# Optimization experiments

Measured on AMD Instinct MI355X. Metric: run time of the kernel, lower is better.

Reference implementation:

```python
import jax, jax.numpy as jnp
import numpy as np

B, R, N, D, H = 32, 5, 1024, 256, 256

def setup_inputs() -> dict:
    key = jax.random.key(0)
    k1, k2, k3, k4 = jax.random.split(key, 4)
    nodes = jax.random.normal(k1, (B, N, D), dtype=jnp.float32)
    adj = jax.random.uniform(k2, (B, R, N, N), dtype=jnp.float32)
    # kaiming_normal_ approximation: std = sqrt(2 / fan_in)
    std = np.sqrt(2.0 / D).astype(np.float32)
    w_0 = jax.random.normal(k3, (H, D), dtype=jnp.float32) * std
    w_r = jax.random.normal(k4, (R, H, D), dtype=jnp.float32) * std
    return {"nodes": nodes, "adj": adj, "w_0": w_0, "w_r": w_r}

def reference(nodes, adj, w_0, w_r):
    # nodes: (B,N,D), adj: (B,R,N,N), w_0: (H,D), w_r: (R,H,D)
    xw_0 = jnp.einsum('bnd,hd->bnh', nodes, w_0)            # (B,N,H)
    xw_r = jnp.einsum('bnd,rhd->brnh', nodes, w_r)          # (B,R,N,H)
    c_r = jnp.sum(adj, axis=-1, keepdims=True)              # (B,R,N,1)
    c_r = jnp.where(c_r == 0, jnp.ones_like(c_r), c_r)
    out = jnp.sum(xw_r / c_r, axis=1) + xw_0                # (B,N,H)
    # dropout is identity in eval mode
    return out
```

## Files before the change

kernel.cpp:

```cpp
#include <hip/hip_runtime.h>
#include <hip/hip_bf16.h>


#define BB 32
#define RR 5
#define NN 1024
#define DD 256
#define HH 256
#define MM (BB * NN)

typedef __attribute__((ext_vector_type(8))) short short8;
typedef __attribute__((ext_vector_type(4))) float f32x4;

#define GAS(p) ((const __attribute__((address_space(1))) void*)(p))
#define LAS(p) ((__attribute__((address_space(3))) void*)(p))

__device__ __forceinline__ unsigned short f2bf(float f) {
    unsigned int u = __float_as_uint(f);
    unsigned int r = (u + 0x7FFFu + ((u >> 16) & 1u)) >> 16;
    return (unsigned short)r;
}

__global__ void cvt_kernel(const float* __restrict__ in,
                           unsigned short* __restrict__ out, int n) {
    int i = (blockIdx.x * blockDim.x + threadIdx.x) * 4;
    if (i >= n) return;
    float4 v = *reinterpret_cast<const float4*>(in + i);
    ushort4 o;
    o.x = f2bf(v.x); o.y = f2bf(v.y); o.z = f2bf(v.z); o.w = f2bf(v.w);
    *reinterpret_cast<ushort4*>(out + i) = o;
}

__global__ __launch_bounds__(256) void rowsum_kernel(const float* __restrict__ adj,
                                                     float* __restrict__ inv_c) {
    const int wave = blockIdx.x * 4 + (threadIdx.x >> 6);
    const int lane = threadIdx.x & 63;
    const float4* row4 = reinterpret_cast<const float4*>(adj + (size_t)wave * NN);
    float s = 0.f;
#pragma unroll
    for (int i = 0; i < 4; ++i) {
        float4 v = row4[lane + 64 * i];
        s += (v.x + v.y) + (v.z + v.w);
    }
#pragma unroll
    for (int off = 32; off > 0; off >>= 1) s += __shfl_down(s, off, 64);
    if (lane == 0) {
        float c = (s == 0.f) ? 1.f : s;
        inv_c[wave] = 1.f / c;
    }
}

__global__ __launch_bounds__(256) void gemm_kernel(
    const unsigned short* __restrict__ nodesb,
    const unsigned short* __restrict__ wb,
    const float* __restrict__ inv_c,
    float* __restrict__ out) {
    __shared__ unsigned short smem[14336];
    __shared__ float s_inv[RR * 64];

    const int tid  = threadIdx.x;
    const int lane = tid & 63;
    const int wv   = tid >> 6;
    const int row_base = blockIdx.x * 64;
    const int col_base = blockIdx.y * 64;
    const int m    = lane & 15;
    const int quad = lane >> 4;

    const unsigned short* gp[7];
    unsigned short*       lp[7];
#pragma unroll
    for (int j = 0; j < 7; ++j) {
        const int c = wv * 7 + j;
        lp[j] = smem + c * 512;
        if (c < 4) {
            const int u   = c * 64 + lane;
            const int row = u >> 2;
            const int kc  = u & 3;
            gp[j] = nodesb + (size_t)(row_base + row) * DD + kc * 8;
        } else {
            const int u    = (c - 4) * 64 + lane;
            const int col6 = u >> 2;
            const int kc   = u & 3;
            const int set  = col6 >> 6;
            const int col  = col6 & 63;
            gp[j] = wb + (size_t)(set * HH + col_base + col) * DD + kc * 8;
        }
    }

    f32x4 acc[6][4];
#pragma unroll
    for (int s = 0; s < 6; ++s)
#pragma unroll
        for (int t = 0; t < 4; ++t) acc[s][t] = (f32x4){0.f, 0.f, 0.f, 0.f};

    const unsigned short* aL = smem + m * 32 + quad * 8;
    const unsigned short* bL = smem + 2048 + (wv * 16 + m) * 32 + quad * 8;

    for (int kt = 0; kt < 8; ++kt) {
        __syncthreads();
#pragma unroll
        for (int j = 0; j < 7; ++j)
            __builtin_amdgcn_global_load_lds(GAS(gp[j] + kt * 32), LAS(lp[j]), 16, 0, 0);
        __syncthreads();

        short8 afr[4];
#pragma unroll
        for (int t = 0; t < 4; ++t)
            afr[t] = *reinterpret_cast<const short8*>(aL + t * 512);
#pragma unroll
        for (int s = 0; s < 6; ++s) {
            short8 bfr = *reinterpret_cast<const short8*>(bL + s * 2048);
#pragma unroll
            for (int t = 0; t < 4; ++t)
                acc[s][t] = __builtin_amdgcn_mfma_f32_16x16x32_bf16(afr[t], bfr, acc[s][t], 0, 0, 0);
        }
    }

    const int b  = row_base >> 10;
    const int n0 = row_base & (NN - 1);
    __syncthreads();
#pragma unroll
    for (int i = tid; i < RR * 64; i += 256) {
        const int r = i >> 6, nl = i & 63;
        s_inv[i] = inv_c[((size_t)b * RR + r) * NN + n0 + nl];
    }
    __syncthreads();

    const int hcol = col_base + wv * 16 + m;
#pragma unroll
    for (int t = 0; t < 4; ++t) {
#pragma unroll
        for (int i = 0; i < 4; ++i) {
            const int rloc = t * 16 + quad * 4 + i;
            float v = acc[0][t][i];
#pragma unroll
            for (int r = 0; r < RR; ++r)
                v += s_inv[r * 64 + rloc] * acc[r + 1][t][i];
            out[(size_t)(row_base + rloc) * HH + hcol] = v;
        }
    }
}

extern "C" void kernel_launch(void* const* d_in, const int* in_sizes, int n_in,
                              void* d_out, int out_size, void* d_ws, size_t ws_size,
                              hipStream_t stream) {
    const float* nodes = (const float*)d_in[0];
    const float* adj   = (const float*)d_in[1];
    const float* w0    = (const float*)d_in[2];
    const float* wr    = (const float*)d_in[3];
    float* out = (float*)d_out;

    unsigned short* nodesb = (unsigned short*)d_ws;
    unsigned short* wb     = (unsigned short*)((char*)d_ws + (size_t)MM * DD * 2);
    float*          inv_c  = (float*)((char*)d_ws + (size_t)MM * DD * 2 + (size_t)6 * HH * DD * 2);

    const int n_nodes = MM * DD;
    const int n_w0    = HH * DD;
    const int n_wr    = RR * HH * DD;

    cvt_kernel<<<n_nodes / 4 / 256, 256, 0, stream>>>(nodes, nodesb, n_nodes);
    cvt_kernel<<<n_w0 / 4 / 256, 256, 0, stream>>>(w0, wb, n_w0);
    cvt_kernel<<<n_wr / 4 / 256, 256, 0, stream>>>(wr, wb + n_w0, n_wr);

    rowsum_kernel<<<(BB * RR * NN) / 4, 256, 0, stream>>>(adj, inv_c);

    gemm_kernel<<<dim3(MM / 64, HH / 64), 256, 0, stream>>>(nodesb, wb, inv_c, out);
}
```

Measured before the change: 904.9 us.

## Fuse prep kernels into one launch and double-buffer GEMM LDS loads

```diff
diff --git a/kernel.cpp b/kernel.cpp
--- a/kernel.cpp
+++ b/kernel.cpp
@@ -8,6 +8,10 @@
 #define DD 256
 #define HH 256
 #define MM (BB * NN)
+
+#define RS_BLOCKS 40960
+#define CVN_BLOCKS 8192
+#define CVW_BLOCKS 384
 
 typedef __attribute__((ext_vector_type(8))) short short8;
 typedef __attribute__((ext_vector_type(4))) float f32x4;
@@ -21,32 +25,42 @@
     return (unsigned short)r;
 }
 
-__global__ void cvt_kernel(const float* __restrict__ in,
-                           unsigned short* __restrict__ out, int n) {
-    int i = (blockIdx.x * blockDim.x + threadIdx.x) * 4;
-    if (i >= n) return;
-    float4 v = *reinterpret_cast<const float4*>(in + i);
-    ushort4 o;
-    o.x = f2bf(v.x); o.y = f2bf(v.y); o.z = f2bf(v.z); o.w = f2bf(v.w);
-    *reinterpret_cast<ushort4*>(out + i) = o;
-}
-
-__global__ __launch_bounds__(256) void rowsum_kernel(const float* __restrict__ adj,
-                                                     float* __restrict__ inv_c) {
-    const int wave = blockIdx.x * 4 + (threadIdx.x >> 6);
-    const int lane = threadIdx.x & 63;
-    const float4* row4 = reinterpret_cast<const float4*>(adj + (size_t)wave * NN);
-    float s = 0.f;
+__global__ __launch_bounds__(256) void prep_kernel(
+    const float* __restrict__ nodes, const float* __restrict__ adj,
+    const float* __restrict__ w0,    const float* __restrict__ wr,
+    unsigned short* __restrict__ nodesb, unsigned short* __restrict__ wb,
+    float* __restrict__ inv_c) {
+    const int bid = blockIdx.x;
+    const int tid = threadIdx.x;
+    if (bid < RS_BLOCKS) {
+        const int wave = bid * 4 + (tid >> 6);
+        const int lane = tid & 63;
+        const float4* row4 = reinterpret_cast<const float4*>(adj + (size_t)wave * NN);
+        float s = 0.f;
 #pragma unroll
-    for (int i = 0; i < 4; ++i) {
-        float4 v = row4[lane + 64 * i];
-        s += (v.x + v.y) + (v.z + v.w);
-    }
+        for (int i = 0; i < 4; ++i) {
+            float4 v = row4[lane + 64 * i];
+            s += (v.x + v.y) + (v.z + v.w);
+        }
 #pragma unroll
-    for (int off = 32; off > 0; off >>= 1) s += __shfl_down(s, off, 64);
-    if (lane == 0) {
-        float c = (s == 0.f) ? 1.f : s;
-        inv_c[wave] = 1.f / c;
+        for (int off = 32; off > 0; off >>= 1) s += __shfl_down(s, off, 64);
+        if (lane == 0) {
+            float c = (s == 0.f) ? 1.f : s;
+            inv_c[wave] = 1.f / c;
+        }
+    } else if (bid < RS_BLOCKS + CVN_BLOCKS) {
+        const int i = ((bid - RS_BLOCKS) * 256 + tid) * 4;
+        float4 v = *reinterpret_cast<const float4*>(nodes + i);
+        ushort4 o;
+        o.x = f2bf(v.x); o.y = f2bf(v.y); o.z = f2bf(v.z); o.w = f2bf(v.w);
+        *reinterpret_cast<ushort4*>(nodesb + i) = o;
+    } else {
+        const int i = ((bid - RS_BLOCKS - CVN_BLOCKS) * 256 + tid) * 4;
+        const float* src = (i < HH * DD) ? (w0 + i) : (wr + (i - HH * DD));
+        float4 v = *reinterpret_cast<const float4*>(src);
+        ushort4 o;
+        o.x = f2bf(v.x); o.y = f2bf(v.y); o.z = f2bf(v.z); o.w = f2bf(v.w);
+        *reinterpret_cast<ushort4*>(wb + i) = o;
     }
 }
 
@@ -55,7 +69,7 @@
     const unsigned short* __restrict__ wb,
     const float* __restrict__ inv_c,
     float* __restrict__ out) {
-    __shared__ unsigned short smem[14336];
+    __shared__ unsigned short smem[2 * 14336];
     __shared__ float s_inv[RR * 64];
 
     const int tid  = threadIdx.x;
@@ -67,11 +81,11 @@
     const int quad = lane >> 4;
 
     const unsigned short* gp[7];
-    unsigned short*       lp[7];
+    int lo[7];
 #pragma unroll
     for (int j = 0; j < 7; ++j) {
         const int c = wv * 7 + j;
-        lp[j] = smem + c * 512;
+        lo[j] = c * 512;
         if (c < 4) {
             const int u   = c * 64 + lane;
             const int row = u >> 2;
@@ -93,16 +107,25 @@
 #pragma unroll
         for (int t = 0; t < 4; ++t) acc[s][t] = (f32x4){0.f, 0.f, 0.f, 0.f};
 
-    const unsigned short* aL = smem + m * 32 + quad * 8;
-    const unsigned short* bL = smem + 2048 + (wv * 16 + m) * 32 + quad * 8;
+    const int aoff = m * 32 + quad * 8;
+    const int boff = 2048 + (wv * 16 + m) * 32 + quad * 8;
 
+#pragma unroll
+    for (int j = 0; j < 7; ++j)
+        __builtin_amdgcn_global_load_lds(GAS(gp[j]), LAS(smem + lo[j]), 16, 0, 0);
+    __syncthreads();
+
+    int cur = 0;
+#pragma unroll
     for (int kt = 0; kt < 8; ++kt) {
-        __syncthreads();
+        if (kt < 7) {
+            unsigned short* nb = smem + (cur ^ 1) * 14336;
 #pragma unroll
-        for (int j = 0; j < 7; ++j)
-            __builtin_amdgcn_global_load_lds(GAS(gp[j] + kt * 32), LAS(lp[j]), 16, 0, 0);
-        __syncthreads();
-
+            for (int j = 0; j < 7; ++j)
+                __builtin_amdgcn_global_load_lds(GAS(gp[j] + (kt + 1) * 32), LAS(nb + lo[j]), 16, 0, 0);
+        }
+        const unsigned short* aL = smem + cur * 14336 + aoff;
+        const unsigned short* bL = smem + cur * 14336 + boff;
         short8 afr[4];
 #pragma unroll
         for (int t = 0; t < 4; ++t)
@@ -114,11 +137,12 @@
             for (int t = 0; t < 4; ++t)
                 acc[s][t] = __builtin_amdgcn_mfma_f32_16x16x32_bf16(afr[t], bfr, acc[s][t], 0, 0, 0);
         }
+        __syncthreads();
+        cur ^= 1;
     }
 
     const int b  = row_base >> 10;
     const int n0 = row_base & (NN - 1);
-    __syncthreads();
 #pragma unroll
     for (int i = tid; i < RR * 64; i += 256) {
         const int r = i >> 6, nl = i & 63;
@@ -154,15 +178,8 @@
     unsigned short* wb     = (unsigned short*)((char*)d_ws + (size_t)MM * DD * 2);
     float*          inv_c  = (float*)((char*)d_ws + (size_t)MM * DD * 2 + (size_t)6 * HH * DD * 2);
 
-    const int n_nodes = MM * DD;
-    const int n_w0    = HH * DD;
-    const int n_wr    = RR * HH * DD;
-
-    cvt_kernel<<<n_nodes / 4 / 256, 256, 0, stream>>>(nodes, nodesb, n_nodes);
-    cvt_kernel<<<n_w0 / 4 / 256, 256, 0, stream>>>(w0, wb, n_w0);
-    cvt_kernel<<<n_wr / 4 / 256, 256, 0, stream>>>(wr, wb + n_w0, n_wr);
-
-    rowsum_kernel<<<(BB * RR * NN) / 4, 256, 0, stream>>>(adj, inv_c);
+    prep_kernel<<<RS_BLOCKS + CVN_BLOCKS + CVW_BLOCKS, 256, 0, stream>>>(
+        nodes, adj, w0, wr, nodesb, wb, inv_c);
 
     gemm_kernel<<<dim3(MM / 64, HH / 64), 256, 0, stream>>>(nodesb, wb, inv_c, out);
 }
```

New measurement: 895.1 us. Within noise of the previous version (-1.1%).
